# Kernel optimization log

Hardware: AMD Instinct MI355X
Metric: run time of the kernel (lower is better)

The kernel has to match this reference:

```python
import jax, jax.numpy as jnp
import numpy as np

NUM_IMU = 72
NUM_NOISE = 12
MAX_PROP = 300
LN_EPS = 1e-5

def _softplus(x):
    return jax.nn.softplus(x)

def setup_inputs() -> dict:
    key = jax.random.key(0)
    k1, k2, k3, k4, k5 = jax.random.split(key, 5)
    d_model = 1024
    seq_len = 4096
    hidden_states = jax.random.normal(k1, (1, seq_len, d_model), dtype=jnp.float32)
    ln_gamma = jnp.ones((d_model,), dtype=jnp.float32)
    ln_beta = jnp.zeros((d_model,), dtype=jnp.float32)
    # Linear: d_model -> NUM_IMU * NUM_NOISE
    W = jax.random.normal(k2, (d_model, NUM_IMU * NUM_NOISE), dtype=jnp.float32) / np.sqrt(d_model)
    b = jax.random.normal(k3, (NUM_IMU * NUM_NOISE,), dtype=jnp.float32) * 0.01
    return {"hidden_states": hidden_states, "ln_gamma": ln_gamma, "ln_beta": ln_beta, "W": W, "b": b}

def _forward(hidden_states, ln_gamma, ln_beta, W, b):
    seq_len = hidden_states.shape[1]
    tsteps = min(MAX_PROP, seq_len)
    x = hidden_states[0]  # [seq, d_model] (squeeze batch=1)
    mu = jnp.mean(x, axis=-1, keepdims=True)
    var = jnp.mean((x - mu) ** 2, axis=-1, keepdims=True)
    xn = (x - mu) * jax.lax.rsqrt(var + LN_EPS) * ln_gamma + ln_beta
    # noise params: [seq, NUM_NOISE, NUM_IMU]
    p = (xn @ W + b).reshape(seq_len, NUM_NOISE, NUM_IMU)
    c = p[:, 4, :]
    c_theta = p[:, 5, :]
    phi = p[:, 6, :]
    phi_theta = p[:, 7, :]
    d = _softplus(p[:, 1, :])
    k = d ** 2 / 4 + _softplus(p[:, 0, :])
    d_theta = _softplus(p[:, 3, :])
    k_theta = d_theta ** 2 / 4 + _softplus(p[:, 2, :])
    acc_base = p[:, 8, :].T      # [imu, seq]
    acc_std = _softplus(p[:, 9, :]).T
    gyro_base = p[:, 10, :].T
    gyro_std = _softplus(p[:, 11, :]).T
    # vectorize over imu: move to [imu, seq, 1]
    def I(a):
        return a.T[:, :, None]
    t = jnp.arange(tsteps, dtype=jnp.float32)[None, None, :]  # [1,1,tstep]
    k_, d_, phi_, c_ = I(k), I(d), I(phi), I(c)
    kt_, dt_, pht_, ct_ = I(k_theta), I(d_theta), I(phi_theta), I(c_theta)
    omega1 = jnp.sqrt(k_ * 4 - d_ ** 2) / 2
    lin = c_ * jnp.exp(-d_ / 2 * t) * jnp.sin(t * omega1 + phi_)
    omega2 = jnp.sqrt(kt_ * 4 - dt_ ** 2) / 2
    ang = ct_ * jnp.exp(-dt_ / 2 * t) * jnp.sin(t * omega2 + pht_)
    spring = lin + ang  # [imu, seq, tstep]
    # banded scatter-add: out[s+t] += spring[:, s, t] for s+t < seq_len
    pos = jnp.arange(seq_len, dtype=jnp.int32)[:, None] + jnp.arange(tsteps, dtype=jnp.int32)[None, :]
    pos_flat = pos.reshape(-1)
    mask = pos_flat < seq_len
    pos_safe = jnp.where(mask, pos_flat, 0)
    vals = spring.reshape(NUM_IMU, -1) * mask.astype(spring.dtype)
    kinematics = jnp.zeros((NUM_IMU, seq_len), dtype=spring.dtype).at[:, pos_safe].add(vals)
    return kinematics, acc_base, acc_std, gyro_base, gyro_std

def reference(hidden_states, ln_gamma, ln_beta, W, b):
    return _forward(hidden_states, ln_gamma, ln_beta, W, b)
```

## Files before the change

### kernel.cpp

```cpp
#include <hip/hip_runtime.h>
#include <hip/hip_bf16.h>
#include <math.h>

#define SEQ 4096
#define DM  1024
#define NIMU 72
#define NNOISE 12
#define NJ (NIMU*NNOISE)
#define TSTEPS 300
#define PLANE (NIMU*SEQ)

#define A2F_SHORTS ((size_t)256 * 64 * 512)
#define BTF_SHORTS ((size_t)56 * 64 * 512)

typedef __attribute__((ext_vector_type(8))) short bf16x8;
typedef __attribute__((ext_vector_type(4))) float f32x4;
typedef __attribute__((ext_vector_type(2))) float f32x2;

__device__ __forceinline__ float softplus_f(float x) {
    return fmaxf(x, 0.f) + log1pf(expf(-fabsf(x)));
}

__device__ __forceinline__ void split_bf16(float x, short& hi, short& lo) {
    unsigned b = __float_as_uint(x);
    unsigned h = (b + 0x7FFFu + ((b >> 16) & 1u)) >> 16;
    float hf = __uint_as_float(h << 16);
    float r = x - hf;
    unsigned b2 = __float_as_uint(r);
    unsigned l2 = (b2 + 0x7FFFu + ((b2 >> 16) & 1u)) >> 16;
    hi = (short)h;
    lo = (short)l2;
}

__global__ __launch_bounds__(256) void ln_kernel(const float* __restrict__ x,
                                                 const float* __restrict__ gamma,
                                                 const float* __restrict__ beta,
                                                 short* __restrict__ A2f) {
    const int s_tile = blockIdx.x;
    const int tid = threadIdx.x;
    const int mrow = tid >> 4;
    const int g    = tid & 15;
    const int row  = s_tile * 16 + mrow;
    const float4* xr = (const float4*)(x + (size_t)row * DM);

    float s = 0.f, sq = 0.f;
    #pragma unroll
    for (int i = 0; i < 16; ++i) {
        float4 v = xr[g + 16 * i];
        s  += v.x + v.y + v.z + v.w;
        sq += v.x*v.x + v.y*v.y + v.z*v.z + v.w*v.w;
    }
    #pragma unroll
    for (int off = 1; off < 16; off <<= 1) {
        s  += __shfl_xor(s, off);
        sq += __shfl_xor(sq, off);
    }
    const float mean = s * (1.f / DM);
    const float var  = sq * (1.f / DM) - mean * mean;
    const float rstd = rsqrtf(fmaxf(var, 0.f) + 1e-5f);

    #pragma unroll
    for (int i = 0; i < 16; ++i) {
        float4 v = xr[g + 16 * i];
        float4 gm = ((const float4*)gamma)[g + 16 * i];
        float4 bt = ((const float4*)beta)[g + 16 * i];
        float o[4];
        o[0] = (v.x - mean) * rstd * gm.x + bt.x;
        o[1] = (v.y - mean) * rstd * gm.y + bt.y;
        o[2] = (v.z - mean) * rstd * gm.z + bt.z;
        o[3] = (v.w - mean) * rstd * gm.w + bt.w;
        short4 hv, lv;
        split_bf16(o[0], hv.x, lv.x);
        split_bf16(o[1], hv.y, lv.y);
        split_bf16(o[2], hv.z, lv.z);
        split_bf16(o[3], hv.w, lv.w);
        const int ch = (g >> 3) + 2 * i;
        const size_t base = ((size_t)s_tile * 64 + ch) * 512
                          + mrow * 8 + ((g >> 1) & 3) * 128 + (g & 1) * 4;
        *(short4*)(A2f + base)             = hv;
        *(short4*)(A2f + base + 32 * 512)  = lv;
    }
}

__global__ __launch_bounds__(256) void wprep_kernel(const float* __restrict__ W,
                                                    short* __restrict__ Btf) {
    __shared__ float T[32][33];
    const int k0 = blockIdx.x * 32, j0 = blockIdx.y * 32;
    const int t = threadIdx.x;
    {
        const int r = t >> 3, c4 = (t & 7) * 4;
        float4 v = *(const float4*)(W + (size_t)(k0 + r) * NJ + j0 + c4);
        T[r][c4 + 0] = v.x; T[r][c4 + 1] = v.y; T[r][c4 + 2] = v.z; T[r][c4 + 3] = v.w;
    }
    __syncthreads();
    if (t < 128) {
        const int gq = t >> 6;
        const int l  = t & 63;
        const int n = l & 15, c = l >> 4;
        const int jt = blockIdx.y * 2 + gq;
        bf16x8 hv, lv;
        #pragma unroll
        for (int o = 0; o < 8; ++o) {
            short h, lo_;
            split_bf16(T[c * 8 + o][gq * 16 + n], h, lo_);
            hv[o] = h; lv[o] = lo_;
        }
        short* dh = Btf + ((size_t)jt * 64 + blockIdx.x) * 512 + l * 8;
        *(bf16x8*)dh = hv;
        *(bf16x8*)(dh + (size_t)32 * 512) = lv;
    }
}

__global__ __launch_bounds__(256, 1) void gemm_kernel(const short* __restrict__ A2f,
                                                      const short* __restrict__ Btf,
                                                      const float* __restrict__ bias,
                                                      float* __restrict__ pt) {
    const int l = threadIdx.x & 63, w = threadIdx.x >> 6;
    const int st0 = blockIdx.x * 8 + (w & 1) * 4;
    const int jt0 = blockIdx.y * 8 + (w >> 1) * 4;
    const short* aB = A2f + (size_t)st0 * (64 * 512) + l * 8;
    const short* bB = Btf + (size_t)jt0 * (64 * 512) + l * 8;

    f32x4 acc[4][4] = {};
    bf16x8 ah[2][4], al[2][4], bh[2][4], bl[2][4];

    auto ldstep = [&](int slot, int i) {
        #pragma unroll
        for (int t = 0; t < 4; ++t) {
            ah[slot][t] = *(const bf16x8*)(aB + ((size_t)t * 64 + i) * 512);
            al[slot][t] = *(const bf16x8*)(aB + ((size_t)t * 64 + 32 + i) * 512);
            bh[slot][t] = *(const bf16x8*)(bB + ((size_t)t * 64 + i) * 512);
            bl[slot][t] = *(const bf16x8*)(bB + ((size_t)t * 64 + 32 + i) * 512);
        }
    };

    ldstep(0, 0);
    #pragma unroll 2
    for (int i = 0; i < 32; ++i) {
        const int cur = i & 1;
        if (i + 1 < 32) ldstep(cur ^ 1, i + 1);
        #pragma unroll
        for (int mi = 0; mi < 4; ++mi)
            #pragma unroll
            for (int ni = 0; ni < 4; ++ni)
                acc[mi][ni] = __builtin_amdgcn_mfma_f32_16x16x32_bf16(
                    ah[cur][mi], bh[cur][ni], acc[mi][ni], 0, 0, 0);
        #pragma unroll
        for (int mi = 0; mi < 4; ++mi)
            #pragma unroll
            for (int ni = 0; ni < 4; ++ni)
                acc[mi][ni] = __builtin_amdgcn_mfma_f32_16x16x32_bf16(
                    ah[cur][mi], bl[cur][ni], acc[mi][ni], 0, 0, 0);
        #pragma unroll
        for (int mi = 0; mi < 4; ++mi)
            #pragma unroll
            for (int ni = 0; ni < 4; ++ni)
                acc[mi][ni] = __builtin_amdgcn_mfma_f32_16x16x32_bf16(
                    al[cur][mi], bh[cur][ni], acc[mi][ni], 0, 0, 0);
    }

    const int srow = (l >> 4) * 4;
    const int jcol = l & 15;
    #pragma unroll
    for (int ni = 0; ni < 4; ++ni) {
        const int j = (jt0 + ni) * 16 + jcol;
        if (j < NJ) {
            const float bj = bias[j];
            #pragma unroll
            for (int mi = 0; mi < 4; ++mi) {
                f32x4 v = acc[mi][ni];
                v[0] += bj; v[1] += bj; v[2] += bj; v[3] += bj;
                *(f32x4*)(pt + (size_t)j * SEQ + (st0 + mi) * 16 + srow) = v;
            }
        }
    }
}

__global__ __launch_bounds__(256) void spring_kernel(const float* __restrict__ pt,
                                                     float* __restrict__ kin) {
    const int tid  = threadIdx.x;
    const int lane = tid & 63;
    const int wid  = tid >> 6;
    const int s0   = blockIdx.x * 256;
    const int imu  = blockIdx.y;
    const int th   = blockIdx.z;
    const int tbeg = th ? 152 : 0;
    const int tlen = th ? 148 : 152;
    const int sbase = s0 + (wid << 6);
    const int s    = sbase + lane;

    const int base = imu * SEQ + s;
    const float p0  = pt[(size_t)0 * PLANE + base];
    const float p1  = pt[(size_t)1 * PLANE + base];
    const float p2  = pt[(size_t)2 * PLANE + base];
    const float p3  = pt[(size_t)3 * PLANE + base];
    const float c1  = pt[(size_t)4 * PLANE + base];
    const float c2  = pt[(size_t)5 * PLANE + base];
    const float ph1 = pt[(size_t)6 * PLANE + base];
    const float ph2 = pt[(size_t)7 * PLANE + base];

    float dd = softplus_f(p1);
    float kk = dd * dd * 0.25f + softplus_f(p0);
    float om1 = 0.5f * sqrtf(fmaxf(4.f * kk - dd * dd, 0.f));
    float dt = softplus_f(p3);
    float kt = dt * dt * 0.25f + softplus_f(p2);
    float om2 = 0.5f * sqrtf(fmaxf(4.f * kt - dt * dt, 0.f));
    float e1 = expf(-0.5f * dd), e2 = expf(-0.5f * dt);
    float sn, cs, sn2, cs2;
    sincosf(om1, &sn, &cs);
    sincosf(om2, &sn2, &cs2);
    f32x2 Rr = {e1 * cs, e2 * cs2};
    f32x2 Ri = {e1 * sn, e2 * sn2};
    sincosf(ph1, &sn, &cs);
    sincosf(ph2, &sn2, &cs2);
    f32x2 zr = {c1 * cs, c2 * cs2};
    f32x2 zi = {c1 * sn, c2 * sn2};

    if (th) {
        f32x2 prr = Rr, pri = Ri;
        f32x2 qr = {1.f, 1.f}, qi = {0.f, 0.f};
        int e = 152;
        while (e) {
            if (e & 1) {
                f32x2 nr = qr * prr - qi * pri;
                qi = qr * pri + qi * prr;
                qr = nr;
            }
            f32x2 nr = prr * prr - pri * pri;
            pri = 2.f * prr * pri;
            prr = nr;
            e >>= 1;
        }
        f32x2 nr = zr * qr - zi * qi;
        zi = zr * qi + zi * qr;
        zr = nr;
    }

    float A[4];
    #pragma unroll
    for (int r = 0; r < 4; ++r) A[r] = 0.f;

    const bool full = (sbase + 63 + tbeg + tlen - 1) < SEQ;

    if (full) {
        #pragma unroll
        for (int tq = 0; tq < 3; ++tq) {
            const int trmax = (tq == 2) ? (tlen - 128) : 64;
            for (int tr0 = 0; tr0 < trmax; tr0 += 4) {
                float v[4], u[4];
                #pragma unroll
                for (int i = 0; i < 4; ++i) {
                    v[i] = zi.x + zi.y;
                    f32x2 nr = zr * Rr - zi * Ri;
                    zi = zr * Ri + zi * Rr;
                    zr = nr;
                }
                #pragma unroll
                for (int i = 0; i < 4; ++i)
                    u[i] = __shfl(v[i], (lane - (tr0 + i)) & 63);
                #pragma unroll
                for (int i = 0; i < 4; ++i) {
                    const int tr = tr0 + i;
                    A[tq]     += (lane >= tr) ? u[i] : 0.f;
                    A[tq + 1] += (lane <  tr) ? u[i] : 0.f;
                }
            }
        }
    } else {
        const int tmax_lane = SEQ - s - tbeg;
        #pragma unroll
        for (int tq = 0; tq < 3; ++tq) {
            const int trmax = (tq == 2) ? (tlen - 128) : 64;
            for (int tr = 0; tr < trmax; ++tr) {
                const int t2 = tq * 64 + tr;
                float val = (t2 < tmax_lane) ? (zi.x + zi.y) : 0.f;
                float u = __shfl(val, (lane - tr) & 63);
                A[tq]     += (lane >= tr) ? u : 0.f;
                A[tq + 1] += (lane <  tr) ? u : 0.f;
                f32x2 nr = zr * Rr - zi * Ri;
                zi = zr * Ri + zi * Rr;
                zr = nr;
            }
        }
    }

    const int pbase = sbase + tbeg;
    #pragma unroll
    for (int r = 0; r < 4; ++r) {
        const int idx = r * 64 + lane;
        if (idx < tlen + 63) {
            const int pos = pbase + idx;
            if (pos < SEQ) {
                __hip_atomic_fetch_add(&kin[(size_t)imu * SEQ + pos], A[r],
                                       __ATOMIC_RELAXED, __HIP_MEMORY_SCOPE_AGENT);
            }
        }
    }
}

__global__ __launch_bounds__(256) void tail_kernel(const float* __restrict__ pt,
                                                   float* __restrict__ out) {
    int idx = blockIdx.x * 256 + threadIdx.x;
    if (idx >= 4 * PLANE) return;
    float v = pt[(size_t)8 * PLANE + idx];
    int q = idx / PLANE;
    if (q & 1) v = softplus_f(v);
    out[(size_t)PLANE + idx] = v;
}

extern "C" void kernel_launch(void* const* d_in, const int* in_sizes, int n_in,
                              void* d_out, int out_size, void* d_ws, size_t ws_size,
                              hipStream_t stream) {
    const float* hs    = (const float*)d_in[0];
    const float* gamma = (const float*)d_in[1];
    const float* beta  = (const float*)d_in[2];
    const float* W     = (const float*)d_in[3];
    const float* b     = (const float*)d_in[4];
    float* out = (float*)d_out;

    short* A2f = (short*)d_ws;
    short* Btf = A2f + A2F_SHORTS;
    float* pt  = (float*)(Btf + BTF_SHORTS);

    hipMemsetAsync(out, 0, (size_t)PLANE * sizeof(float), stream);

    ln_kernel<<<SEQ / 16, 256, 0, stream>>>(hs, gamma, beta, A2f);
    wprep_kernel<<<dim3(DM / 32, NJ / 32), 256, 0, stream>>>(W, Btf);
    gemm_kernel<<<dim3(SEQ / 128, 7), 256, 0, stream>>>(A2f, Btf, b, pt);
    spring_kernel<<<dim3(SEQ / 256, NIMU, 2), 256, 0, stream>>>(pt, out);
    tail_kernel<<<(4 * PLANE + 255) / 256, 256, 0, stream>>>(pt, out);
}
```

Baseline: 159.7 us.

## Accumulate spring band in shared-memory window via LDS atomics

Replaces the wave-shuffle banded reduction and the two-way time split with one block per (seq tile, imu). Each thread walks all 300 timesteps and does LDS atomic adds into a 555-float shared window, which is then flushed to global memory with agent-scope atomics. This drops the shuffle and select work, the complex power-by-squaring prefix and the masked edge path, but it issues 300 LDS atomics per thread and halves the grid, which may reduce parallelism. Out-of-range positions are dropped at flush time.

```diff
diff --git a/kernel.cpp b/kernel.cpp
--- a/kernel.cpp
+++ b/kernel.cpp
@@ -178,16 +178,14 @@
 
 __global__ __launch_bounds__(256) void spring_kernel(const float* __restrict__ pt,
                                                      float* __restrict__ kin) {
-    const int tid  = threadIdx.x;
-    const int lane = tid & 63;
-    const int wid  = tid >> 6;
-    const int s0   = blockIdx.x * 256;
-    const int imu  = blockIdx.y;
-    const int th   = blockIdx.z;
-    const int tbeg = th ? 152 : 0;
-    const int tlen = th ? 148 : 152;
-    const int sbase = s0 + (wid << 6);
-    const int s    = sbase + lane;
+    __shared__ float win[560];
+    const int tid = threadIdx.x;
+    const int s0  = blockIdx.x * 256;
+    const int imu = blockIdx.y;
+    const int s   = s0 + tid;
+
+    #pragma unroll
+    for (int i = tid; i < 555; i += 256) win[i] = 0.f;
 
     const int base = imu * SEQ + s;
     const float p0  = pt[(size_t)0 * PLANE + base];
@@ -216,84 +214,25 @@
     f32x2 zr = {c1 * cs, c2 * cs2};
     f32x2 zi = {c1 * sn, c2 * sn2};
 
-    if (th) {
-        f32x2 prr = Rr, pri = Ri;
-        f32x2 qr = {1.f, 1.f}, qi = {0.f, 0.f};
-        int e = 152;
-        while (e) {
-            if (e & 1) {
-                f32x2 nr = qr * prr - qi * pri;
-                qi = qr * pri + qi * prr;
-                qr = nr;
-            }
-            f32x2 nr = prr * prr - pri * pri;
-            pri = 2.f * prr * pri;
-            prr = nr;
-            e >>= 1;
-        }
-        f32x2 nr = zr * qr - zi * qi;
-        zi = zr * qi + zi * qr;
+    __syncthreads();
+
+    float* wp = &win[tid];
+    #pragma unroll 10
+    for (int t = 0; t < TSTEPS; ++t) {
+        const float val = zi.x + zi.y;
+        (void)__hip_atomic_fetch_add(wp + t, val,
+                                     __ATOMIC_RELAXED, __HIP_MEMORY_SCOPE_WORKGROUP);
+        f32x2 nr = zr * Rr - zi * Ri;
+        zi = zr * Ri + zi * Rr;
         zr = nr;
     }
 
-    float A[4];
-    #pragma unroll
-    for (int r = 0; r < 4; ++r) A[r] = 0.f;
-
-    const bool full = (sbase + 63 + tbeg + tlen - 1) < SEQ;
-
-    if (full) {
-        #pragma unroll
-        for (int tq = 0; tq < 3; ++tq) {
-            const int trmax = (tq == 2) ? (tlen - 128) : 64;
-            for (int tr0 = 0; tr0 < trmax; tr0 += 4) {
-                float v[4], u[4];
-                #pragma unroll
-                for (int i = 0; i < 4; ++i) {
-                    v[i] = zi.x + zi.y;
-                    f32x2 nr = zr * Rr - zi * Ri;
-                    zi = zr * Ri + zi * Rr;
-                    zr = nr;
-                }
-                #pragma unroll
-                for (int i = 0; i < 4; ++i)
-                    u[i] = __shfl(v[i], (lane - (tr0 + i)) & 63);
-                #pragma unroll
-                for (int i = 0; i < 4; ++i) {
-                    const int tr = tr0 + i;
-                    A[tq]     += (lane >= tr) ? u[i] : 0.f;
-                    A[tq + 1] += (lane <  tr) ? u[i] : 0.f;
-                }
-            }
-        }
-    } else {
-        const int tmax_lane = SEQ - s - tbeg;
-        #pragma unroll
-        for (int tq = 0; tq < 3; ++tq) {
-            const int trmax = (tq == 2) ? (tlen - 128) : 64;
-            for (int tr = 0; tr < trmax; ++tr) {
-                const int t2 = tq * 64 + tr;
-                float val = (t2 < tmax_lane) ? (zi.x + zi.y) : 0.f;
-                float u = __shfl(val, (lane - tr) & 63);
-                A[tq]     += (lane >= tr) ? u : 0.f;
-                A[tq + 1] += (lane <  tr) ? u : 0.f;
-                f32x2 nr = zr * Rr - zi * Ri;
-                zi = zr * Ri + zi * Rr;
-                zr = nr;
-            }
-        }
-    }
-
-    const int pbase = sbase + tbeg;
-    #pragma unroll
-    for (int r = 0; r < 4; ++r) {
-        const int idx = r * 64 + lane;
-        if (idx < tlen + 63) {
-            const int pos = pbase + idx;
-            if (pos < SEQ) {
-                __hip_atomic_fetch_add(&kin[(size_t)imu * SEQ + pos], A[r],
-                                       __ATOMIC_RELAXED, __HIP_MEMORY_SCOPE_AGENT);
-            }
+    __syncthreads();
+    for (int i = tid; i < 555; i += 256) {
+        const int pos = s0 + i;
+        if (pos < SEQ) {
+            (void)__hip_atomic_fetch_add(&kin[(size_t)imu * SEQ + pos], win[i],
+                                         __ATOMIC_RELAXED, __HIP_MEMORY_SCOPE_AGENT);
         }
     }
 }
@@ -327,6 +266,6 @@
     ln_kernel<<<SEQ / 16, 256, 0, stream>>>(hs, gamma, beta, A2f);
     wprep_kernel<<<dim3(DM / 32, NJ / 32), 256, 0, stream>>>(W, Btf);
     gemm_kernel<<<dim3(SEQ / 128, 7), 256, 0, stream>>>(A2f, Btf, b, pt);
-    spring_kernel<<<dim3(SEQ / 256, NIMU, 2), 256, 0, stream>>>(pt, out);
+    spring_kernel<<<dim3(SEQ / 256, NIMU), 256, 0, stream>>>(pt, out);
     tail_kernel<<<(4 * PLANE + 255) / 256, 256, 0, stream>>>(pt, out);
 }
```

Result: slower. 610.3 us (+282.1%).
